# Optimization experiments

Hardware: AMD Instinct MI355X
Metric: run time of the kernel (lower is better)

The kernel has to match this reference:

```python
import jax, jax.numpy as jnp
import numpy as np

ALPHA = 0.3


def _maxsim_scores(q, d):
    # q: [B, N, D], d: [C, S, D] -> scores [B, C]
    # MaxSim: per (query b, doc c), sum over query tokens of max over doc tokens.
    sim = jnp.einsum('bnd,csd->bcns', q, d)  # [B, C, N, S]
    return sim.max(axis=3).sum(axis=2)       # [B, C]


def setup_inputs() -> dict:
    key = jax.random.key(0)
    k1, k2, k3, k4 = jax.random.split(key, 4)
    B, N, S, D = 64, 32, 1024, 128
    return {
        'query_embeddings': jax.random.normal(k1, (B, N, D), dtype=jnp.float32),
        'doc_embeddings': jax.random.normal(k2, (B, S, D), dtype=jnp.float32),
        'teacher_query_outputs': jax.random.normal(k3, (B, N, D), dtype=jnp.float32),
        'teacher_doc_outputs': jax.random.normal(k4, (B, S, D), dtype=jnp.float32),
    }


def reference(query_embeddings, doc_embeddings, teacher_query_outputs, teacher_doc_outputs):
    scores = _maxsim_scores(query_embeddings, doc_embeddings)  # [B, B]
    B = scores.shape[0]
    pos_scores = jnp.diag(scores)                               # [B]
    eye = jnp.eye(B, dtype=bool)
    s_masked = jnp.where(eye, -jnp.inf, scores)
    neg_scores = s_masked.max(axis=1)                           # hardest negative per query
    contrastive_loss = jax.nn.softplus(neg_scores - pos_scores).mean()

    teacher_scores = _maxsim_scores(teacher_query_outputs, teacher_doc_outputs)
    # Torch MSELoss on fp16-cast inputs: compute in fp16, then promote.
    diff16 = scores.astype(jnp.float16) - teacher_scores.astype(jnp.float16)
    mse_loss = jnp.mean(diff16 * diff16).astype(jnp.float32)

    return contrastive_loss + ALPHA * mse_loss
```

## Files before the change

kernel.cpp:

```cpp
#include <hip/hip_runtime.h>
#include <hip/hip_bf16.h>

typedef __attribute__((ext_vector_type(8))) short short8;
typedef __attribute__((ext_vector_type(4))) float floatx4;

#define B_SZ   64
#define N_TOK  32
#define S_TOK  1024
#define D_DIM  128
#define ALPHA  0.3f

#define STRIP_S     32
#define STRIP_EL    (STRIP_S * D_DIM)
#define STRIP_BYTES (STRIP_EL * 2)
#define NSTRIP      (S_TOK / STRIP_S)
#define C_EL        (S_TOK * D_DIM)

__device__ __forceinline__ short f2bf(float f) {
    __hip_bfloat16 h = __float2bfloat16(f);
    return __builtin_bit_cast(short, h);
}

__device__ __forceinline__ short8 cvt8(const float* __restrict__ p) {
    floatx4 f0 = *reinterpret_cast<const floatx4*>(p);
    floatx4 f1 = *reinterpret_cast<const floatx4*>(p + 4);
    short8 r;
    r[0] = f2bf(f0[0]); r[1] = f2bf(f0[1]); r[2] = f2bf(f0[2]); r[3] = f2bf(f0[3]);
    r[4] = f2bf(f1[0]); r[5] = f2bf(f1[1]); r[6] = f2bf(f1[2]); r[7] = f2bf(f1[3]);
    return r;
}

__global__ __launch_bounds__(256) void cvt_q_kernel(
    const float* __restrict__ q, const float* __restrict__ tq,
    __hip_bfloat16* __restrict__ qb, __hip_bfloat16* __restrict__ tqb) {
    const float* src = blockIdx.y ? tq : q;
    __hip_bfloat16* dst = blockIdx.y ? tqb : qb;
    int idx = blockIdx.x * 256 + threadIdx.x;
    *reinterpret_cast<short8*>(dst + (size_t)idx * 8) = cvt8(src + (size_t)idx * 8);
}

__global__ __launch_bounds__(256) void cvt_d_kernel(
    const float* __restrict__ d, const float* __restrict__ td,
    __hip_bfloat16* __restrict__ db, __hip_bfloat16* __restrict__ tdb) {
    const float* src = blockIdx.y ? td : d;
    __hip_bfloat16* dst = blockIdx.y ? tdb : db;
    int idx = blockIdx.x * 256 + threadIdx.x;
    int kc = idx & 15;
    int s  = (idx >> 4) & (S_TOK - 1);
    int c  = idx >> 14;
    int st = s >> 5, nt = (s >> 4) & 1, lr = s & 15;
    int ks = kc >> 2, lg = kc & 3;
    size_t dpos = (size_t)c * C_EL + (size_t)st * STRIP_EL
                + (size_t)(ks * 2 + nt) * 512 + (size_t)(lg * 16 + lr) * 8;
    *reinterpret_cast<short8*>(dst + dpos) = cvt8(src + (size_t)idx * 8);
}

__device__ __forceinline__ void gload_lds16(const void* g, void* l) {
    __builtin_amdgcn_global_load_lds(
        (const __attribute__((address_space(1))) unsigned int*)g,
        (__attribute__((address_space(3))) unsigned int*)l, 16, 0, 0);
}

__global__ __launch_bounds__(256, 4) void maxsim_scores_kernel(
    const __hip_bfloat16* __restrict__ qb,  const __hip_bfloat16* __restrict__ db,
    const __hip_bfloat16* __restrict__ tqb, const __hip_bfloat16* __restrict__ tdb,
    float* __restrict__ scores_ws ) {

    const int c     = blockIdx.x;
    const int bg    = blockIdx.y;
    const int which = blockIdx.z;
    const __hip_bfloat16* Q = which ? tqb : qb;
    const __hip_bfloat16* D = which ? tdb : db;
    float* out = scores_ws + which * (B_SZ * B_SZ);

    const int tid = threadIdx.x;
    const int w   = tid >> 6;
    const int l   = tid & 63;
    const int lg  = l >> 4;
    const int lr  = l & 15;

    const int b0 = bg * 8 + w * 2;

    __shared__ __align__(16) char smem[2 * STRIP_BYTES];

    short8 afrag[4][4];
#pragma unroll
    for (int mt = 0; mt < 4; ++mt)
#pragma unroll
        for (int ks = 0; ks < 4; ++ks)
            afrag[mt][ks] = *reinterpret_cast<const short8*>(
                Q + ((size_t)(b0 + (mt >> 1)) * N_TOK + (mt & 1) * 16 + lr) * D_DIM
                  + ks * 32 + lg * 8);

    float runmax[4][4];
#pragma unroll
    for (int mt = 0; mt < 4; ++mt)
#pragma unroll
        for (int j = 0; j < 4; ++j) runmax[mt][j] = -INFINITY;

    const char* gstrip = (const char*)(D + (size_t)c * C_EL);
    const unsigned y0 = tid * 16;
    const unsigned y1 = 4096 + tid * 16;

    gload_lds16(gstrip + y0, smem + y0);
    gload_lds16(gstrip + y1, smem + y1);
    __syncthreads();

    for (int st = 0; st < NSTRIP; ++st) {
        const char* bufc = smem + (size_t)(st & 1) * STRIP_BYTES;

        if (st + 1 < NSTRIP) {
            const char* gs = gstrip + (size_t)(st + 1) * STRIP_BYTES;
            char* bufn = smem + (size_t)((st + 1) & 1) * STRIP_BYTES;
            gload_lds16(gs + y0, bufn + y0);
            gload_lds16(gs + y1, bufn + y1);
        }

#pragma unroll
        for (int nt = 0; nt < 2; ++nt) {
            short8 bf[4];
#pragma unroll
            for (int ks = 0; ks < 4; ++ks)
                bf[ks] = *reinterpret_cast<const short8*>(
                    bufc + (ks * 2 + nt) * 1024 + l * 16);

            floatx4 acc[4];
#pragma unroll
            for (int mt = 0; mt < 4; ++mt) acc[mt] = floatx4{0.f, 0.f, 0.f, 0.f};

#pragma unroll
            for (int ks = 0; ks < 4; ++ks)
#pragma unroll
                for (int mt = 0; mt < 4; ++mt)
                    acc[mt] = __builtin_amdgcn_mfma_f32_16x16x32_bf16(
                        afrag[mt][ks], bf[ks], acc[mt], 0, 0, 0);

#pragma unroll
            for (int mt = 0; mt < 4; ++mt)
#pragma unroll
                for (int j = 0; j < 4; ++j)
                    runmax[mt][j] = fmaxf(runmax[mt][j], acc[mt][j]);
        }

        __syncthreads();
    }

#pragma unroll
    for (int mt = 0; mt < 4; ++mt)
#pragma unroll
        for (int j = 0; j < 4; ++j) {
            float v = runmax[mt][j];
            v = fmaxf(v, __shfl_xor(v, 1));
            v = fmaxf(v, __shfl_xor(v, 2));
            v = fmaxf(v, __shfl_xor(v, 4));
            v = fmaxf(v, __shfl_xor(v, 8));
            runmax[mt][j] = v;
        }

    float s0 = 0.f, s1 = 0.f;
#pragma unroll
    for (int j = 0; j < 4; ++j) {
        s0 += runmax[0][j] + runmax[1][j];
        s1 += runmax[2][j] + runmax[3][j];
    }
    s0 += __shfl_xor(s0, 16); s0 += __shfl_xor(s0, 32);
    s1 += __shfl_xor(s1, 16); s1 += __shfl_xor(s1, 32);

    if (l == 0) {
        out[b0 * B_SZ + c]       = s0;
        out[(b0 + 1) * B_SZ + c] = s1;
    }
}

__global__ void loss_kernel(const float* __restrict__ scores_ws, float* __restrict__ out) {
    const float* sc = scores_ws;
    const float* tc = scores_ws + B_SZ * B_SZ;
    const int b = threadIdx.x;

    float pos = sc[b * B_SZ + b];
    float neg = -INFINITY;
    float msesum = 0.f;
#pragma unroll 8
    for (int cc = 0; cc < B_SZ; ++cc) {
        float s = sc[b * B_SZ + cc];
        float t = tc[b * B_SZ + cc];
        if (cc != b) neg = fmaxf(neg, s);
        _Float16 d16 = (_Float16)s - (_Float16)t;
        _Float16 sq  = d16 * d16;
        msesum += (float)sq;
    }
    float x = neg - pos;
    float sp = (x > 0.f) ? (x + log1pf(expf(-x))) : log1pf(expf(x));

#pragma unroll
    for (int m = 1; m < 64; m <<= 1) {
        sp     += __shfl_xor(sp, m);
        msesum += __shfl_xor(msesum, m);
    }
    if (b == 0) {
        float mse = msesum / 4096.f;
        mse = (float)(_Float16)mse;
        out[0] = sp / 64.f + ALPHA * mse;
    }
}

extern "C" void kernel_launch(void* const* d_in, const int* in_sizes, int n_in,
                              void* d_out, int out_size, void* d_ws, size_t ws_size,
                              hipStream_t stream) {
    const float* q  = (const float*)d_in[0];
    const float* d  = (const float*)d_in[1];
    const float* tq = (const float*)d_in[2];
    const float* td = (const float*)d_in[3];
    float* out = (float*)d_out;

    const size_t QN = (size_t)B_SZ * N_TOK * D_DIM;
    const size_t DN = (size_t)B_SZ * S_TOK * D_DIM;

    float* scores_ws = (float*)d_ws;
    __hip_bfloat16* qb  = (__hip_bfloat16*)((char*)d_ws + 32768);
    __hip_bfloat16* tqb = qb + QN;
    __hip_bfloat16* db  = tqb + QN;
    __hip_bfloat16* tdb = db + DN;

    cvt_q_kernel<<<dim3((unsigned)(QN / 8 / 256), 2), 256, 0, stream>>>(q, tq, qb, tqb);
    cvt_d_kernel<<<dim3((unsigned)(DN / 8 / 256), 2), 256, 0, stream>>>(d, td, db, tdb);

    dim3 grid(B_SZ, B_SZ / 8, 2);
    maxsim_scores_kernel<<<grid, 256, 0, stream>>>(qb, db, tqb, tdb, scores_ws);
    loss_kernel<<<1, 64, 0, stream>>>(scores_ws, out);
}
```

Measured before the change: 80.17 us.

## Double query rows per block to halve doc reloads; merge conversion kernels

Each block of the maxsim kernel now covers 16 queries instead of 8, so every streamed document strip feeds twice as many MFMAs and total doc-strip traffic from global/L2 is halved. The grid shrinks from 1024 to 512 blocks and launch bounds drop to 2 blocks per CU to make room for the doubled A-fragment and running-max registers. The two bf16 conversion kernels are merged into one launch to save a kernel launch. The risks are lower occupancy and fewer blocks per CU to hide latency.

New measurement: 73.98 us. -7.7%, faster.

```diff
diff --git a/kernel.cpp b/kernel.cpp
--- a/kernel.cpp
+++ b/kernel.cpp
@@ -15,6 +15,9 @@
 #define STRIP_BYTES (STRIP_EL * 2)
 #define NSTRIP      (S_TOK / STRIP_S)
 #define C_EL        (S_TOK * D_DIM)
+
+#define DBLK (B_SZ * S_TOK * D_DIM / 8 / 256)
+#define QBLK (B_SZ * N_TOK * D_DIM / 8 / 256)
 
 __device__ __forceinline__ short f2bf(float f) {
     __hip_bfloat16 h = __float2bfloat16(f);
@@ -30,29 +33,30 @@
     return r;
 }
 
-__global__ __launch_bounds__(256) void cvt_q_kernel(
-    const float* __restrict__ q, const float* __restrict__ tq,
-    __hip_bfloat16* __restrict__ qb, __hip_bfloat16* __restrict__ tqb) {
-    const float* src = blockIdx.y ? tq : q;
-    __hip_bfloat16* dst = blockIdx.y ? tqb : qb;
-    int idx = blockIdx.x * 256 + threadIdx.x;
-    *reinterpret_cast<short8*>(dst + (size_t)idx * 8) = cvt8(src + (size_t)idx * 8);
-}
-
-__global__ __launch_bounds__(256) void cvt_d_kernel(
-    const float* __restrict__ d, const float* __restrict__ td,
-    __hip_bfloat16* __restrict__ db, __hip_bfloat16* __restrict__ tdb) {
-    const float* src = blockIdx.y ? td : d;
-    __hip_bfloat16* dst = blockIdx.y ? tdb : db;
-    int idx = blockIdx.x * 256 + threadIdx.x;
-    int kc = idx & 15;
-    int s  = (idx >> 4) & (S_TOK - 1);
-    int c  = idx >> 14;
-    int st = s >> 5, nt = (s >> 4) & 1, lr = s & 15;
-    int ks = kc >> 2, lg = kc & 3;
-    size_t dpos = (size_t)c * C_EL + (size_t)st * STRIP_EL
-                + (size_t)(ks * 2 + nt) * 512 + (size_t)(lg * 16 + lr) * 8;
-    *reinterpret_cast<short8*>(dst + dpos) = cvt8(src + (size_t)idx * 8);
+__global__ __launch_bounds__(256) void cvt_all_kernel(
+    const float* __restrict__ q,  const float* __restrict__ d,
+    const float* __restrict__ tq, const float* __restrict__ td,
+    __hip_bfloat16* __restrict__ qb,  __hip_bfloat16* __restrict__ db,
+    __hip_bfloat16* __restrict__ tqb, __hip_bfloat16* __restrict__ tdb) {
+    const int which = blockIdx.y;
+    if (blockIdx.x >= DBLK) {
+        const float* src = which ? tq : q;
+        __hip_bfloat16* dst = which ? tqb : qb;
+        int idx = (blockIdx.x - DBLK) * 256 + threadIdx.x;
+        *reinterpret_cast<short8*>(dst + (size_t)idx * 8) = cvt8(src + (size_t)idx * 8);
+    } else {
+        const float* src = which ? td : d;
+        __hip_bfloat16* dst = which ? tdb : db;
+        int idx = blockIdx.x * 256 + threadIdx.x;
+        int kc = idx & 15;
+        int s  = (idx >> 4) & (S_TOK - 1);
+        int c  = idx >> 14;
+        int st = s >> 5, nt = (s >> 4) & 1, lr = s & 15;
+        int ks = kc >> 2, lg = kc & 3;
+        size_t dpos = (size_t)c * C_EL + (size_t)st * STRIP_EL
+                    + (size_t)(ks * 2 + nt) * 512 + (size_t)(lg * 16 + lr) * 8;
+        *reinterpret_cast<short8*>(dst + dpos) = cvt8(src + (size_t)idx * 8);
+    }
 }
 
 __device__ __forceinline__ void gload_lds16(const void* g, void* l) {
@@ -61,7 +65,7 @@
         (__attribute__((address_space(3))) unsigned int*)l, 16, 0, 0);
 }
 
-__global__ __launch_bounds__(256, 4) void maxsim_scores_kernel(
+__global__ __launch_bounds__(256, 2) void maxsim_scores_kernel(
     const __hip_bfloat16* __restrict__ qb,  const __hip_bfloat16* __restrict__ db,
     const __hip_bfloat16* __restrict__ tqb, const __hip_bfloat16* __restrict__ tdb,
     float* __restrict__ scores_ws ) {
@@ -79,22 +83,22 @@
     const int lg  = l >> 4;
     const int lr  = l & 15;
 
-    const int b0 = bg * 8 + w * 2;
+    const int b0 = bg * 16 + w * 4;
 
     __shared__ __align__(16) char smem[2 * STRIP_BYTES];
 
-    short8 afrag[4][4];
-#pragma unroll
-    for (int mt = 0; mt < 4; ++mt)
+    short8 afrag[8][4];
+#pragma unroll
+    for (int mt = 0; mt < 8; ++mt)
 #pragma unroll
         for (int ks = 0; ks < 4; ++ks)
             afrag[mt][ks] = *reinterpret_cast<const short8*>(
                 Q + ((size_t)(b0 + (mt >> 1)) * N_TOK + (mt & 1) * 16 + lr) * D_DIM
                   + ks * 32 + lg * 8);
 
-    float runmax[4][4];
-#pragma unroll
-    for (int mt = 0; mt < 4; ++mt)
+    float runmax[8][4];
+#pragma unroll
+    for (int mt = 0; mt < 8; ++mt)
 #pragma unroll
         for (int j = 0; j < 4; ++j) runmax[mt][j] = -INFINITY;
 
@@ -124,19 +128,19 @@
                 bf[ks] = *reinterpret_cast<const short8*>(
                     bufc + (ks * 2 + nt) * 1024 + l * 16);
 
-            floatx4 acc[4];
-#pragma unroll
-            for (int mt = 0; mt < 4; ++mt) acc[mt] = floatx4{0.f, 0.f, 0.f, 0.f};
+            floatx4 acc[8];
+#pragma unroll
+            for (int mt = 0; mt < 8; ++mt) acc[mt] = floatx4{0.f, 0.f, 0.f, 0.f};
 
 #pragma unroll
             for (int ks = 0; ks < 4; ++ks)
 #pragma unroll
-                for (int mt = 0; mt < 4; ++mt)
+                for (int mt = 0; mt < 8; ++mt)
                     acc[mt] = __builtin_amdgcn_mfma_f32_16x16x32_bf16(
                         afrag[mt][ks], bf[ks], acc[mt], 0, 0, 0);
 
 #pragma unroll
-            for (int mt = 0; mt < 4; ++mt)
+            for (int mt = 0; mt < 8; ++mt)
 #pragma unroll
                 for (int j = 0; j < 4; ++j)
                     runmax[mt][j] = fmaxf(runmax[mt][j], acc[mt][j]);
@@ -146,7 +150,7 @@
     }
 
 #pragma unroll
-    for (int mt = 0; mt < 4; ++mt)
+    for (int mt = 0; mt < 8; ++mt)
 #pragma unroll
         for (int j = 0; j < 4; ++j) {
             float v = runmax[mt][j];
@@ -157,18 +161,14 @@
             runmax[mt][j] = v;
         }
 
-    float s0 = 0.f, s1 = 0.f;
-#pragma unroll
-    for (int j = 0; j < 4; ++j) {
-        s0 += runmax[0][j] + runmax[1][j];
-        s1 += runmax[2][j] + runmax[3][j];
-    }
-    s0 += __shfl_xor(s0, 16); s0 += __shfl_xor(s0, 32);
-    s1 += __shfl_xor(s1, 16); s1 += __shfl_xor(s1, 32);
-
-    if (l == 0) {
-        out[b0 * B_SZ + c]       = s0;
-        out[(b0 + 1) * B_SZ + c] = s1;
+#pragma unroll
+    for (int p = 0; p < 4; ++p) {
+        float s = 0.f;
+#pragma unroll
+        for (int j = 0; j < 4; ++j) s += runmax[2 * p][j] + runmax[2 * p + 1][j];
+        s += __shfl_xor(s, 16);
+        s += __shfl_xor(s, 32);
+        if (l == 0) out[(b0 + p) * B_SZ + c] = s;
     }
 }
 
@@ -222,10 +222,10 @@
     __hip_bfloat16* db  = tqb + QN;
     __hip_bfloat16* tdb = db + DN;
 
-    cvt_q_kernel<<<dim3((unsigned)(QN / 8 / 256), 2), 256, 0, stream>>>(q, tq, qb, tqb);
-    cvt_d_kernel<<<dim3((unsigned)(DN / 8 / 256), 2), 256, 0, stream>>>(d, td, db, tdb);
-
-    dim3 grid(B_SZ, B_SZ / 8, 2);
+    cvt_all_kernel<<<dim3(DBLK + QBLK, 2), 256, 0, stream>>>(
+        q, d, tq, td, qb, db, tqb, tdb);
+
+    dim3 grid(B_SZ, B_SZ / 16, 2);
     maxsim_scores_kernel<<<grid, 256, 0, stream>>>(qb, db, tqb, tdb, scores_ws);
     loss_kernel<<<1, 64, 0, stream>>>(scores_ws, out);
 }
```
